# Kernel optimization log

Measured on AMD Instinct MI355X. Metric: run time of the kernel, lower is better.

Reference implementation:

```python
import jax, jax.numpy as jnp
import numpy as np

N = 100000        # nodes
E = 1600000       # edges (before self-loops)
IN_DIM = 3
HID = 64
OUT = 74          # 3 + 71
MLP_HID = 128
NEG_SLOPE = 0.2


def setup_inputs() -> dict:
    key = jax.random.key(0)
    ks = jax.random.split(key, 16)
    g = lambda k, shape, fan: (jax.random.normal(k, shape, jnp.float32) / np.sqrt(fan)).astype(jnp.float32)
    return {
        "x": jax.random.normal(ks[0], (N, IN_DIM), jnp.float32),
        "edge_index": jax.random.randint(ks[1], (2, E), 0, N, jnp.int32),
        # GAT layer 1 (heads=1): linear weight, attention vectors, bias
        "W1": g(ks[2], (IN_DIM, HID), IN_DIM),
        "a1_src": g(ks[3], (HID,), HID),
        "a1_dst": g(ks[4], (HID,), HID),
        "b1": jnp.zeros((HID,), jnp.float32),
        # GAT layer 2
        "W2": g(ks[5], (HID, HID), HID),
        "a2_src": g(ks[6], (HID,), HID),
        "a2_dst": g(ks[7], (HID,), HID),
        "b2": jnp.zeros((HID,), jnp.float32),
        # policy head MLP
        "Wp1": g(ks[8], (HID, MLP_HID), HID),
        "bp1": jnp.zeros((MLP_HID,), jnp.float32),
        "Wp2": g(ks[9], (MLP_HID, OUT), MLP_HID),
        "bp2": jnp.zeros((OUT,), jnp.float32),
    }


def gat_layer(x, W, a_src, a_dst, b, src, dst):
    # PyG GATConv, heads=1: h = x W; e_ij = LeakyReLU(a_src.h_j + a_dst.h_i)
    h = x @ W                                   # [N, HID]
    e = jax.nn.leaky_relu((h @ a_src)[src] + (h @ a_dst)[dst], NEG_SLOPE)  # [E']
    m = jax.lax.stop_gradient(jax.ops.segment_max(e, dst, num_segments=N))
    p = jnp.exp(e - m[dst])
    s = jax.ops.segment_sum(p, dst, num_segments=N)
    alpha = p / s[dst]                          # softmax over incoming edges
    out = jax.ops.segment_sum(alpha[:, None] * h[src], dst, num_segments=N)
    return out + b


def reference(x, edge_index, W1, a1_src, a1_dst, b1, W2, a2_src, a2_dst, b2, Wp1, bp1, Wp2, bp2):
    # add self-loops (PyG GATConv default add_self_loops=True)
    loops = jnp.arange(N, dtype=edge_index.dtype)
    src = jnp.concatenate([edge_index[0], loops])
    dst = jnp.concatenate([edge_index[1], loops])
    x = jax.nn.relu(gat_layer(x, W1, a1_src, a1_dst, b1, src, dst))
    x = jax.nn.relu(gat_layer(x, W2, a2_src, a2_dst, b2, src, dst))
    h = jax.nn.relu(x @ Wp1 + bp1)
    return h @ Wp2 + bp2
```

## Files before the change

kernel.cpp:

```cpp
#include <hip/hip_runtime.h>
#include <math.h>

#define NN   100000
#define EE   1600000
#define ET   (EE + NN)
#define HID  64
#define MLPH 128
#define ODIM 74
#define SLOPE 0.2f

#define NB   196
#define GA   800
#define EPB  (EE / GA)

__device__ __forceinline__ float f4get(const float4& v, int i) {
    return i == 0 ? v.x : i == 1 ? v.y : i == 2 ? v.z : v.w;
}
__device__ __forceinline__ unsigned short f2bf(float f) {
    unsigned u = __float_as_uint(f);
    u += 0x7fffu + ((u >> 16) & 1u);
    return (unsigned short)(u >> 16);
}
__device__ __forceinline__ float bf2f(unsigned short s) {
    return __uint_as_float(((unsigned)s) << 16);
}


__global__ void k_partA_hist(const int* __restrict__ edst, int* __restrict__ M) {
    __shared__ int hist[NB];
    int t = threadIdx.x;
    if (t < NB) hist[t] = 0;
    __syncthreads();
    int base = blockIdx.x * EPB;
    for (int i = t; i < EPB; i += 256)
        atomicAdd(&hist[edst[base + i] >> 9], 1);
    __syncthreads();
    if (t < NB) M[blockIdx.x * NB + t] = hist[t];
}

__global__ void k_scan_col(const int* __restrict__ M, int* __restrict__ colExcl,
                           int* __restrict__ colsum) {
    __shared__ int sd[256];
    __shared__ int carry;
    int k = blockIdx.x, t = threadIdx.x;
    if (t == 0) carry = 0;
    __syncthreads();
    for (int c = 0; c < GA; c += 256) {
        int v = (c + t < GA) ? M[(c + t) * NB + k] : 0;
        sd[t] = v;
        __syncthreads();
        for (int o = 1; o < 256; o <<= 1) {
            int u = (t >= o) ? sd[t - o] : 0;
            __syncthreads();
            sd[t] += u;
            __syncthreads();
        }
        if (c + t < GA) colExcl[(c + t) * NB + k] = carry + sd[t] - v;
        __syncthreads();
        if (t == 255) carry += sd[255];
        __syncthreads();
    }
    if (t == 0) colsum[k] = carry;
}

__global__ void k_scan_bkt(const int* __restrict__ colsum, int* __restrict__ bucketBase) {
    __shared__ int sd[256];
    int t = threadIdx.x;
    int v = (t < NB) ? colsum[t] : 0;
    sd[t] = v;
    __syncthreads();
    for (int o = 1; o < 256; o <<= 1) {
        int u = (t >= o) ? sd[t - o] : 0;
        __syncthreads();
        sd[t] += u;
        __syncthreads();
    }
    if (t < NB) bucketBase[t] = sd[t] - v;
    if (t == NB - 1) bucketBase[NB] = sd[t];
}

__global__ void k_partA_scat(const int* __restrict__ esrc, const int* __restrict__ edst,
                             const int* __restrict__ colExcl, const int* __restrict__ bucketBase,
                             unsigned long long* __restrict__ tmp) {
    __shared__ int cur[NB];
    int t = threadIdx.x;
    if (t < NB) cur[t] = bucketBase[t] + colExcl[blockIdx.x * NB + t];
    __syncthreads();
    int base = blockIdx.x * EPB;
    for (int i = t; i < EPB; i += 256) {
        int s = esrc[base + i], d = edst[base + i];
        int pos = atomicAdd(&cur[d >> 9], 1);
        tmp[pos] = ((unsigned long long)(unsigned)d << 32) | (unsigned)s;
    }
}

__global__ __launch_bounds__(512) void k_partB(
        const unsigned long long* __restrict__ tmp, const int* __restrict__ bucketBase,
        int* __restrict__ rowbeg, int* __restrict__ rowend, int* __restrict__ col) {
    __shared__ int deg[512];
    __shared__ int rb[512];
    __shared__ int cur[512];
    int k = blockIdx.x, t = threadIdx.x;
    int lo = bucketBase[k], hi = bucketBase[k + 1];
    int nodeBase = k << 9;
    int nNodes = (NN - nodeBase < 512) ? (NN - nodeBase) : 512;

    deg[t] = 0;
    __syncthreads();
    for (int i = lo + t; i < hi; i += 512)
        atomicAdd(&deg[(int)(tmp[i] >> 32) - nodeBase], 1);
    __syncthreads();

    int v = (t < nNodes) ? deg[t] + 1 : 0;
    rb[t] = v;
    __syncthreads();
    for (int o = 1; o < 512; o <<= 1) {
        int u = (t >= o) ? rb[t - o] : 0;
        __syncthreads();
        rb[t] += u;
        __syncthreads();
    }
    int myBeg = lo + nodeBase + rb[t] - v;
    if (t < nNodes) {
        int g = nodeBase + t;
        rowbeg[g] = myBeg;
        rowend[g] = myBeg + deg[t] + 1;
        col[myBeg] = g;
        cur[t] = myBeg + 1;
    }
    __syncthreads();
    for (int i = lo + t; i < hi; i += 512) {
        unsigned long long e = tmp[i];
        int dLow = (int)(e >> 32) - nodeBase;
        int pos = atomicAdd(&cur[dLow], 1);
        col[pos] = (int)(e & 0xffffffffu);
    }
}


__global__ void k_lin1(const float* __restrict__ x, const float* __restrict__ W,
                       const float* __restrict__ asrc, const float* __restrict__ adst,
                       unsigned short* __restrict__ h16,
                       float* __restrict__ hs, float* __restrict__ hd) {
    int node = blockIdx.x * 4 + (threadIdx.x >> 6);
    int f    = threadIdx.x & 63;
    float x0 = x[node*3+0], x1 = x[node*3+1], x2 = x[node*3+2];
    float v  = x0*W[f] + x1*W[64+f] + x2*W[128+f];
    h16[node*64+f] = f2bf(v);
    float ps = v*asrc[f], pd = v*adst[f];
    #pragma unroll
    for (int o = 32; o > 0; o >>= 1) { ps += __shfl_down(ps, o); pd += __shfl_down(pd, o); }
    if (f == 0) { hs[node] = ps; hd[node] = pd; }
}

__global__ __launch_bounds__(128) void k_lin64(
        const float* __restrict__ xin, const float* __restrict__ W,
        const float* __restrict__ asrc, const float* __restrict__ adst,
        unsigned short* __restrict__ h16,
        float* __restrict__ hs, float* __restrict__ hd) {
    __shared__ __align__(16) float xr[32][64];
    __shared__ __align__(16) float wl[64*64];
    int t  = threadIdx.x;
    int nb = blockIdx.x * 32;
    for (int i = t; i < 32*64; i += 128) xr[i >> 6][i & 63] = xin[nb*64 + i];
    for (int i = t; i < 64*64;  i += 128) wl[i] = W[i];
    __syncthreads();

    int nq = t >> 4;
    int hq = t & 15;
    float acc[4][4] = {};
    #pragma unroll 4
    for (int k = 0; k < 64; k += 4) {
        float4 xv[4];
        #pragma unroll
        for (int ni = 0; ni < 4; ++ni) xv[ni] = *(const float4*)&xr[nq*4+ni][k];
        #pragma unroll
        for (int kk = 0; kk < 4; ++kk) {
            float4 wv = *(const float4*)&wl[(k+kk)*64 + hq*4];
            #pragma unroll
            for (int ni = 0; ni < 4; ++ni) {
                float xs = f4get(xv[ni], kk);
                acc[ni][0] += xs*wv.x; acc[ni][1] += xs*wv.y;
                acc[ni][2] += xs*wv.z; acc[ni][3] += xs*wv.w;
            }
        }
    }
    float4 res[4];
    #pragma unroll
    for (int ni = 0; ni < 4; ++ni) {
        res[ni] = make_float4(acc[ni][0], acc[ni][1], acc[ni][2], acc[ni][3]);
        ushort4 u4;
        u4.x = f2bf(res[ni].x); u4.y = f2bf(res[ni].y);
        u4.z = f2bf(res[ni].z); u4.w = f2bf(res[ni].w);
        *(ushort4*)&h16[(size_t)(nb + nq*4 + ni)*64 + hq*4] = u4;
    }
    __syncthreads();
    #pragma unroll
    for (int ni = 0; ni < 4; ++ni) *(float4*)&xr[nq*4+ni][hq*4] = res[ni];
    __syncthreads();

    int wv_  = t >> 6;
    int lane = t & 63;
    for (int ni = 0; ni < 16; ++ni) {
        int node = wv_*16 + ni;
        float v  = xr[node][lane];
        float ps = v*asrc[lane], pd = v*adst[lane];
        #pragma unroll
        for (int o = 32; o > 0; o >>= 1) { ps += __shfl_down(ps, o); pd += __shfl_down(pd, o); }
        if (lane == 0) { hs[nb+node] = ps; hd[nb+node] = pd; }
    }
}

__global__ void k_gat(const int* __restrict__ rowbeg, const int* __restrict__ rowend,
                      const int* __restrict__ col,
                      const float* __restrict__ hs, const float* __restrict__ hd,
                      const unsigned short* __restrict__ h16, const float* __restrict__ bias,
                      float* __restrict__ out) {
    __shared__ float se[4][128];
    __shared__ int   sc[4][128];
    int w    = threadIdx.x >> 6;
    int lane = threadIdx.x & 63;
    int n    = blockIdx.x * 4 + w;
    float* e_ = se[w];
    int*   c_ = sc[w];

    int base = rowbeg[n];
    int d    = rowend[n] - base;
    float hdn = hd[n];

    float mymax = -INFINITY;
    for (int k = lane; k < d; k += 64) {
        int s = col[base + k];
        float scv = hs[s] + hdn;
        scv = (scv > 0.f) ? scv : SLOPE * scv;
        if (k < 128) { e_[k] = scv; c_[k] = s; }
        mymax = fmaxf(mymax, scv);
    }
    #pragma unroll
    for (int o = 32; o > 0; o >>= 1) mymax = fmaxf(mymax, __shfl_xor(mymax, o));

    float mysum = 0.f;
    for (int k = lane; k < d; k += 64) {
        float scv;
        if (k < 128) scv = e_[k];
        else {
            int s = col[base + k];
            scv = hs[s] + hdn;
            scv = (scv > 0.f) ? scv : SLOPE * scv;
        }
        float p = expf(scv - mymax);
        if (k < 128) e_[k] = p;
        mysum += p;
    }
    #pragma unroll
    for (int o = 32; o > 0; o >>= 1) mysum += __shfl_xor(mysum, o);
    float inv = 1.f / mysum;

    __syncthreads();

    int g = lane >> 4;
    int q = lane & 15;
    int dl = (d < 128) ? d : 128;
    float4 acc4 = make_float4(0.f, 0.f, 0.f, 0.f);
    int k = g;
    for (; k + 4 < dl; k += 8) {
        float p0 = e_[k];     int s0 = c_[k];
        float p1 = e_[k+4];   int s1 = c_[k+4];
        ushort4 u0 = *(const ushort4*)&h16[(size_t)s0*64 + q*4];
        ushort4 u1 = *(const ushort4*)&h16[(size_t)s1*64 + q*4];
        acc4.x += p0*bf2f(u0.x) + p1*bf2f(u1.x);
        acc4.y += p0*bf2f(u0.y) + p1*bf2f(u1.y);
        acc4.z += p0*bf2f(u0.z) + p1*bf2f(u1.z);
        acc4.w += p0*bf2f(u0.w) + p1*bf2f(u1.w);
    }
    if (k < dl) {
        float p0 = e_[k];     int s0 = c_[k];
        ushort4 u0 = *(const ushort4*)&h16[(size_t)s0*64 + q*4];
        acc4.x += p0*bf2f(u0.x); acc4.y += p0*bf2f(u0.y);
        acc4.z += p0*bf2f(u0.z); acc4.w += p0*bf2f(u0.w);
    }
    for (int kk = 128 + g; kk < d; kk += 4) {
        int s = col[base + kk];
        float scv = hs[s] + hdn;
        scv = (scv > 0.f) ? scv : SLOPE * scv;
        float p = expf(scv - mymax);
        ushort4 u0 = *(const ushort4*)&h16[(size_t)s*64 + q*4];
        acc4.x += p*bf2f(u0.x); acc4.y += p*bf2f(u0.y);
        acc4.z += p*bf2f(u0.z); acc4.w += p*bf2f(u0.w);
    }
    #pragma unroll
    for (int o = 16; o <= 32; o <<= 1) {
        acc4.x += __shfl_xor(acc4.x, o);
        acc4.y += __shfl_xor(acc4.y, o);
        acc4.z += __shfl_xor(acc4.z, o);
        acc4.w += __shfl_xor(acc4.w, o);
    }
    if (g == 0) {
        float4 bv = *(const float4*)&bias[q*4];
        float4 r;
        r.x = fmaxf(acc4.x*inv + bv.x, 0.f);
        r.y = fmaxf(acc4.y*inv + bv.y, 0.f);
        r.z = fmaxf(acc4.z*inv + bv.z, 0.f);
        r.w = fmaxf(acc4.w*inv + bv.w, 0.f);
        *(float4*)&out[(size_t)n*64 + q*4] = r;
    }
}

__global__ __launch_bounds__(256) void k_mlp(
        const float* __restrict__ xin,
        const float* __restrict__ Wp1, const float* __restrict__ bp1,
        const float* __restrict__ Wp2, const float* __restrict__ bp2,
        float* __restrict__ out) {
    __shared__ __align__(16) float xr[32][64];
    __shared__ __align__(16) float hid[32][132];
    int t  = threadIdx.x;
    int nb = blockIdx.x * 32;
    int nq = t >> 5;
    int hq = t & 31;

    for (int i = t; i < 32*64; i += 256) xr[i >> 6][i & 63] = xin[(size_t)nb*64 + i];
    __syncthreads();

    {
        float4 bv = *(const float4*)&bp1[hq*4];
        float acc[4][4];
        #pragma unroll
        for (int ni = 0; ni < 4; ++ni) {
            acc[ni][0] = bv.x; acc[ni][1] = bv.y; acc[ni][2] = bv.z; acc[ni][3] = bv.w;
        }
        #pragma unroll 2
        for (int k = 0; k < 64; k += 4) {
            float4 xv[4];
            #pragma unroll
            for (int ni = 0; ni < 4; ++ni) xv[ni] = *(const float4*)&xr[nq*4+ni][k];
            #pragma unroll
            for (int kk = 0; kk < 4; ++kk) {
                float4 wv = *(const float4*)&Wp1[(k+kk)*MLPH + hq*4];
                #pragma unroll
                for (int ni = 0; ni < 4; ++ni) {
                    float xs = f4get(xv[ni], kk);
                    acc[ni][0] += xs*wv.x; acc[ni][1] += xs*wv.y;
                    acc[ni][2] += xs*wv.z; acc[ni][3] += xs*wv.w;
                }
            }
        }
        #pragma unroll
        for (int ni = 0; ni < 4; ++ni)
            *(float4*)&hid[nq*4+ni][hq*4] = make_float4(
                fmaxf(acc[ni][0], 0.f), fmaxf(acc[ni][1], 0.f),
                fmaxf(acc[ni][2], 0.f), fmaxf(acc[ni][3], 0.f));
    }
    __syncthreads();

    {
        int oq = t & 31;
        bool has3 = (oq + 64) < ODIM;
        float a0[4], a1[4], a2[4];
        float b0 = bp2[oq], b1v = bp2[oq+32], b2v = has3 ? bp2[oq+64] : 0.f;
        #pragma unroll
        for (int ni = 0; ni < 4; ++ni) { a0[ni] = b0; a1[ni] = b1v; a2[ni] = b2v; }
        #pragma unroll 2
        for (int j = 0; j < MLPH; j += 4) {
            float4 hv[4];
            #pragma unroll
            for (int ni = 0; ni < 4; ++ni) hv[ni] = *(const float4*)&hid[nq*4+ni][j];
            #pragma unroll
            for (int jj = 0; jj < 4; ++jj) {
                float w0 = Wp2[(j+jj)*ODIM + oq];
                float w1 = Wp2[(j+jj)*ODIM + oq + 32];
                float w2 = has3 ? Wp2[(j+jj)*ODIM + oq + 64] : 0.f;
                float h0 = f4get(hv[0], jj), h1 = f4get(hv[1], jj);
                float h2 = f4get(hv[2], jj), h3 = f4get(hv[3], jj);
                a0[0] += h0*w0; a1[0] += h0*w1; a2[0] += h0*w2;
                a0[1] += h1*w0; a1[1] += h1*w1; a2[1] += h1*w2;
                a0[2] += h2*w0; a1[2] += h2*w1; a2[2] += h2*w2;
                a0[3] += h3*w0; a1[3] += h3*w1; a2[3] += h3*w2;
            }
        }
        #pragma unroll
        for (int ni = 0; ni < 4; ++ni) {
            size_t rowo = (size_t)(nb + nq*4 + ni) * ODIM;
            out[rowo + oq]      = a0[ni];
            out[rowo + oq + 32] = a1[ni];
            if (has3) out[rowo + oq + 64] = a2[ni];
        }
    }
}


extern "C" void kernel_launch(void* const* d_in, const int* in_sizes, int n_in,
                              void* d_out, int out_size, void* d_ws, size_t ws_size,
                              hipStream_t stream) {
    const float* x    = (const float*)d_in[0];
    const int*   ei   = (const int*)  d_in[1];
    const float* W1   = (const float*)d_in[2];
    const float* a1s  = (const float*)d_in[3];
    const float* a1d  = (const float*)d_in[4];
    const float* b1   = (const float*)d_in[5];
    const float* W2   = (const float*)d_in[6];
    const float* a2s  = (const float*)d_in[7];
    const float* a2d  = (const float*)d_in[8];
    const float* b2   = (const float*)d_in[9];
    const float* Wp1  = (const float*)d_in[10];
    const float* bp1  = (const float*)d_in[11];
    const float* Wp2  = (const float*)d_in[12];
    const float* bp2  = (const float*)d_in[13];
    float* out = (float*)d_out;

    const int* esrc = ei;
    const int* edst = ei + EE;

    float* ws   = (float*)d_ws;
    float* bufA = ws;
    float* bufB = bufA + NN*HID;
    float* hs   = bufB + NN*HID;
    float* hd   = hs + NN;
    int* rowbeg = (int*)(hd + NN);
    int* rowend = rowbeg + NN;
    int* col    = rowend + NN;
    int* M      = col + ET;
    int* colExcl= M + GA*NB;
    int* colsum = colExcl + GA*NB;
    int* bucketBase = colsum + NB;
    unsigned long long* tmp = (unsigned long long*)bufA;
    unsigned short* h16 = (unsigned short*)bufA;

    k_partA_hist<<<GA, 256, 0, stream>>>(edst, M);
    k_scan_col  <<<NB, 256, 0, stream>>>(M, colExcl, colsum);
    k_scan_bkt  <<<1, 256, 0, stream>>>(colsum, bucketBase);
    k_partA_scat<<<GA, 256, 0, stream>>>(esrc, edst, colExcl, bucketBase, tmp);
    k_partB     <<<NB, 512, 0, stream>>>(tmp, bucketBase, rowbeg, rowend, col);

    k_lin1<<<NN/4, 256, 0, stream>>>(x, W1, a1s, a1d, h16, hs, hd);
    k_gat <<<NN/4, 256, 0, stream>>>(rowbeg, rowend, col, hs, hd, h16, b1, bufB);

    k_lin64<<<NN/32, 128, 0, stream>>>(bufB, W2, a2s, a2d, h16, hs, hd);
    k_gat  <<<NN/4, 256, 0, stream>>>(rowbeg, rowend, col, hs, hd, h16, b2, bufB);

    k_mlp<<<NN/32, 256, 0, stream>>>(bufB, Wp1, bp1, Wp2, bp2, out);
}
```

Measured before the change: 377.0 us.

## Run policy-head MLP on bf16 MFMA with prepacked weight fragments

Measured after the change: 320.7 us. -14.9%, faster.

```diff
diff --git a/kernel.cpp b/kernel.cpp
--- a/kernel.cpp
+++ b/kernel.cpp
@@ -12,6 +12,9 @@
 #define NB   196
 #define GA   800
 #define EPB  (EE / GA)
+
+typedef __attribute__((ext_vector_type(8))) short bf16x8;
+typedef __attribute__((ext_vector_type(4))) float f32x4;
 
 __device__ __forceinline__ float f4get(const float4& v, int i) {
     return i == 0 ? v.x : i == 1 ? v.y : i == 2 ? v.z : v.w;
@@ -134,6 +137,21 @@
         int dLow = (int)(e >> 32) - nodeBase;
         int pos = atomicAdd(&cur[dLow], 1);
         col[pos] = (int)(e & 0xffffffffu);
+    }
+}
+
+__global__ void k_prepw(const float* __restrict__ Wp1, const float* __restrict__ Wp2,
+                        unsigned short* __restrict__ w1p, unsigned short* __restrict__ w2p) {
+    int i = blockIdx.x * 256 + threadIdx.x;
+    if (i < 8192) {
+        int e = i & 7, lane = (i >> 3) & 63, kb = (i >> 9) & 1, nt = i >> 10;
+        int k = kb*32 + ((lane >> 4) << 3) + e, n = nt*16 + (lane & 15);
+        w1p[i] = f2bf(Wp1[k*MLPH + n]);
+    }
+    if (i < 12288) {
+        int e = i & 7, lane = (i >> 3) & 63, kb = (i >> 9) & 3, nt = i >> 11;
+        int k = kb*32 + ((lane >> 4) << 3) + e, n = nt*16 + (lane & 15);
+        w2p[i] = (n < ODIM) ? f2bf(Wp2[k*ODIM + n]) : (unsigned short)0;
     }
 }
 
@@ -308,81 +326,75 @@
 
 __global__ __launch_bounds__(256) void k_mlp(
         const float* __restrict__ xin,
-        const float* __restrict__ Wp1, const float* __restrict__ bp1,
-        const float* __restrict__ Wp2, const float* __restrict__ bp2,
+        const unsigned short* __restrict__ w1p, const float* __restrict__ bp1,
+        const unsigned short* __restrict__ w2p, const float* __restrict__ bp2,
         float* __restrict__ out) {
-    __shared__ __align__(16) float xr[32][64];
-    __shared__ __align__(16) float hid[32][132];
+    __shared__ __align__(16) unsigned short x16[32][72];
+    __shared__ __align__(16) unsigned short hid16[32][136];
     int t  = threadIdx.x;
     int nb = blockIdx.x * 32;
-    int nq = t >> 5;
-    int hq = t & 31;
-
-    for (int i = t; i < 32*64; i += 256) xr[i >> 6][i & 63] = xin[(size_t)nb*64 + i];
-    __syncthreads();
 
     {
-        float4 bv = *(const float4*)&bp1[hq*4];
-        float acc[4][4];
-        #pragma unroll
-        for (int ni = 0; ni < 4; ++ni) {
-            acc[ni][0] = bv.x; acc[ni][1] = bv.y; acc[ni][2] = bv.z; acc[ni][3] = bv.w;
+        int r = t >> 3, c = (t & 7) * 8;
+        float4 v0 = *(const float4*)&xin[(size_t)(nb + r)*64 + c];
+        float4 v1 = *(const float4*)&xin[(size_t)(nb + r)*64 + c + 4];
+        ushort4 u0, u1;
+        u0.x = f2bf(v0.x); u0.y = f2bf(v0.y); u0.z = f2bf(v0.z); u0.w = f2bf(v0.w);
+        u1.x = f2bf(v1.x); u1.y = f2bf(v1.y); u1.z = f2bf(v1.z); u1.w = f2bf(v1.w);
+        *(ushort4*)&x16[r][c]     = u0;
+        *(ushort4*)&x16[r][c + 4] = u1;
+    }
+    __syncthreads();
+
+    int w = t >> 6, lane = t & 63;
+    int lrow = lane & 15;
+    int lk   = (lane >> 4) * 8;
+    int lr4  = (lane >> 4) * 4;
+
+    {
+        int mt  = w >> 1;
+        int ntb = (w & 1) * 4;
+        bf16x8 a0 = *(const bf16x8*)&x16[mt*16 + lrow][lk];
+        bf16x8 a1 = *(const bf16x8*)&x16[mt*16 + lrow][32 + lk];
+        #pragma unroll
+        for (int j = 0; j < 4; ++j) {
+            int nt = ntb + j;
+            float bv = bp1[nt*16 + lrow];
+            f32x4 acc = { bv, bv, bv, bv };
+            bf16x8 b0 = *(const bf16x8*)&w1p[(size_t)((nt*2 + 0)*64 + lane)*8];
+            bf16x8 b1 = *(const bf16x8*)&w1p[(size_t)((nt*2 + 1)*64 + lane)*8];
+            acc = __builtin_amdgcn_mfma_f32_16x16x32_bf16(a0, b0, acc, 0, 0, 0);
+            acc = __builtin_amdgcn_mfma_f32_16x16x32_bf16(a1, b1, acc, 0, 0, 0);
+            #pragma unroll
+            for (int r = 0; r < 4; ++r)
+                hid16[mt*16 + lr4 + r][nt*16 + lrow] = f2bf(fmaxf(acc[r], 0.f));
         }
-        #pragma unroll 2
-        for (int k = 0; k < 64; k += 4) {
-            float4 xv[4];
+    }
+    __syncthreads();
+
+    {
+        int mt  = w >> 1;
+        int ntb = (w & 1) * 3;
+        bf16x8 a[4];
+        #pragma unroll
+        for (int kb = 0; kb < 4; ++kb)
+            a[kb] = *(const bf16x8*)&hid16[mt*16 + lrow][kb*32 + lk];
+        #pragma unroll
+        for (int j = 0; j < 3; ++j) {
+            int nt = ntb + j;
+            int n  = nt*16 + lrow;
+            float bv = (n < ODIM) ? bp2[n] : 0.f;
+            f32x4 acc = { bv, bv, bv, bv };
             #pragma unroll
-            for (int ni = 0; ni < 4; ++ni) xv[ni] = *(const float4*)&xr[nq*4+ni][k];
-            #pragma unroll
-            for (int kk = 0; kk < 4; ++kk) {
-                float4 wv = *(const float4*)&Wp1[(k+kk)*MLPH + hq*4];
+            for (int kb = 0; kb < 4; ++kb) {
+                bf16x8 b = *(const bf16x8*)&w2p[(size_t)((nt*4 + kb)*64 + lane)*8];
+                acc = __builtin_amdgcn_mfma_f32_16x16x32_bf16(a[kb], b, acc, 0, 0, 0);
+            }
+            if (n < ODIM) {
                 #pragma unroll
-                for (int ni = 0; ni < 4; ++ni) {
-                    float xs = f4get(xv[ni], kk);
-                    acc[ni][0] += xs*wv.x; acc[ni][1] += xs*wv.y;
-                    acc[ni][2] += xs*wv.z; acc[ni][3] += xs*wv.w;
-                }
+                for (int r = 0; r < 4; ++r)
+                    out[(size_t)(nb + mt*16 + lr4 + r)*ODIM + n] = acc[r];
             }
-        }
-        #pragma unroll
-        for (int ni = 0; ni < 4; ++ni)
-            *(float4*)&hid[nq*4+ni][hq*4] = make_float4(
-                fmaxf(acc[ni][0], 0.f), fmaxf(acc[ni][1], 0.f),
-                fmaxf(acc[ni][2], 0.f), fmaxf(acc[ni][3], 0.f));
-    }
-    __syncthreads();
-
-    {
-        int oq = t & 31;
-        bool has3 = (oq + 64) < ODIM;
-        float a0[4], a1[4], a2[4];
-        float b0 = bp2[oq], b1v = bp2[oq+32], b2v = has3 ? bp2[oq+64] : 0.f;
-        #pragma unroll
-        for (int ni = 0; ni < 4; ++ni) { a0[ni] = b0; a1[ni] = b1v; a2[ni] = b2v; }
-        #pragma unroll 2
-        for (int j = 0; j < MLPH; j += 4) {
-            float4 hv[4];
-            #pragma unroll
-            for (int ni = 0; ni < 4; ++ni) hv[ni] = *(const float4*)&hid[nq*4+ni][j];
-            #pragma unroll
-            for (int jj = 0; jj < 4; ++jj) {
-                float w0 = Wp2[(j+jj)*ODIM + oq];
-                float w1 = Wp2[(j+jj)*ODIM + oq + 32];
-                float w2 = has3 ? Wp2[(j+jj)*ODIM + oq + 64] : 0.f;
-                float h0 = f4get(hv[0], jj), h1 = f4get(hv[1], jj);
-                float h2 = f4get(hv[2], jj), h3 = f4get(hv[3], jj);
-                a0[0] += h0*w0; a1[0] += h0*w1; a2[0] += h0*w2;
-                a0[1] += h1*w0; a1[1] += h1*w1; a2[1] += h1*w2;
-                a0[2] += h2*w0; a1[2] += h2*w1; a2[2] += h2*w2;
-                a0[3] += h3*w0; a1[3] += h3*w1; a2[3] += h3*w2;
-            }
-        }
-        #pragma unroll
-        for (int ni = 0; ni < 4; ++ni) {
-            size_t rowo = (size_t)(nb + nq*4 + ni) * ODIM;
-            out[rowo + oq]      = a0[ni];
-            out[rowo + oq + 32] = a1[ni];
-            if (has3) out[rowo + oq + 64] = a2[ni];
         }
     }
 }
@@ -422,6 +434,8 @@
     int* colExcl= M + GA*NB;
     int* colsum = colExcl + GA*NB;
     int* bucketBase = colsum + NB;
+    unsigned short* w1p = (unsigned short*)(bucketBase + 200);
+    unsigned short* w2p = w1p + 8192;
     unsigned long long* tmp = (unsigned long long*)bufA;
     unsigned short* h16 = (unsigned short*)bufA;
 
@@ -430,6 +444,7 @@
     k_scan_bkt  <<<1, 256, 0, stream>>>(colsum, bucketBase);
     k_partA_scat<<<GA, 256, 0, stream>>>(esrc, edst, colExcl, bucketBase, tmp);
     k_partB     <<<NB, 512, 0, stream>>>(tmp, bucketBase, rowbeg, rowend, col);
+    k_prepw     <<<48, 256, 0, stream>>>(Wp1, Wp2, w1p, w2p);
 
     k_lin1<<<NN/4, 256, 0, stream>>>(x, W1, a1s, a1d, h16, hs, hd);
     k_gat <<<NN/4, 256, 0, stream>>>(rowbeg, rowend, col, hs, hd, h16, b1, bufB);
@@ -437,5 +452,5 @@
     k_lin64<<<NN/32, 128, 0, stream>>>(bufB, W2, a2s, a2d, h16, hs, hd);
     k_gat  <<<NN/4, 256, 0, stream>>>(rowbeg, rowend, col, hs, hd, h16, b2, bufB);
 
-    k_mlp<<<NN/32, 256, 0, stream>>>(bufB, Wp1, bp1, Wp2, bp2, out);
-}
+    k_mlp<<<NN/32, 256, 0, stream>>>(bufB, w1p, bp1, w2p, bp2, out);
+}
```
